# Kernel optimization log

Hardware: AMD Instinct MI355X
Metric: run time of the kernel (lower is better)

Reference implementation:

```python
import jax, jax.numpy as jnp
import numpy as np

C = 256
G = 32  # GroupNorm groups
EPS = 1e-6


def setup_inputs() -> dict:
    key = jax.random.key(0)
    ks = jax.random.split(key, 10)
    b, c, d, h, w = 2, C, 16, 16, 16
    s = 1.0 / np.sqrt(c)
    return {
        "x": jax.random.normal(ks[0], (b, c, d, h, w), jnp.float32),
        "gn_gamma": jnp.ones((c,), jnp.float32),
        "gn_beta": jnp.zeros((c,), jnp.float32),
        "wq": jax.random.normal(ks[1], (c, c), jnp.float32) * s,
        "bq": jax.random.normal(ks[2], (c,), jnp.float32) * 0.01,
        "wk": jax.random.normal(ks[3], (c, c), jnp.float32) * s,
        "bk": jax.random.normal(ks[4], (c,), jnp.float32) * 0.01,
        "wv": jax.random.normal(ks[5], (c, c), jnp.float32) * s,
        "bv": jax.random.normal(ks[6], (c,), jnp.float32) * 0.01,
        "wp": jax.random.normal(ks[7], (c, c), jnp.float32) * s,
        "bp": jax.random.normal(ks[8], (c,), jnp.float32) * 0.01,
    }


def _group_norm(x, gamma, beta):
    b, c, d, h, w = x.shape
    xg = x.reshape(b, G, c // G, d, h, w)
    mu = jnp.mean(xg, axis=(2, 3, 4, 5), keepdims=True)
    var = jnp.var(xg, axis=(2, 3, 4, 5), keepdims=True)
    xn = ((xg - mu) * jax.lax.rsqrt(var + EPS)).reshape(b, c, d, h, w)
    return xn * gamma[None, :, None, None, None] + beta[None, :, None, None, None]


def reference(x, gn_gamma, gn_beta, wq, bq, wk, bk, wv, bv, wp, bp):
    b, c, d, h, w = x.shape
    n = d * h * w
    hn = _group_norm(x, gn_gamma, gn_beta).reshape(b, c, n)  # (b, c, n)
    # 1x1 conv3d == channel-mixing matmul
    q = jnp.einsum("oc,bcn->bon", wq, hn) + bq[None, :, None]
    k = jnp.einsum("oc,bcn->bon", wk, hn) + bk[None, :, None]
    v = jnp.einsum("oc,bcn->bon", wv, hn) + bv[None, :, None]
    scale = c ** (-0.5)
    attn = jax.nn.softmax(jnp.einsum("bcn,bcm->bnm", q, k) * scale, axis=2)  # (b, n, m)
    # torch: h_ = bmm(v, attn^T) -> h_[b,c,n] = sum_m v[b,c,m] * attn[b,n,m]
    hv = jnp.einsum("bcm,bnm->bcn", v, attn)
    out = jnp.einsum("oc,bcn->bon", wp, hv) + bp[None, :, None]
    w_returned = jnp.transpose(attn, (0, 2, 1))  # matches torch's returned permuted w_
    return (x + out.reshape(b, c, d, h, w), w_returned)
```

## Files before the change

kernel.cpp:

```cpp
#include <hip/hip_runtime.h>


typedef __bf16 bf16_t;
typedef __bf16 bf16x8 __attribute__((ext_vector_type(8)));
typedef float floatx4 __attribute__((ext_vector_type(4)));

__device__ __forceinline__ unsigned short f2bf(float f) {
  union { float f; unsigned int u; } v; v.f = f;
  return (unsigned short)((v.u + 0x7FFFu + ((v.u >> 16) & 1u)) >> 16);
}
__device__ __forceinline__ float bf2f(unsigned short u) {
  union { unsigned int u; float f; } v; v.u = ((unsigned int)u) << 16;
  return v.f;
}

__global__ void conv_w_kernel(const float* __restrict__ w0, const float* __restrict__ w1,
                              const float* __restrict__ w2, const float* __restrict__ w3,
                              unsigned short* __restrict__ dst) {
  const float* src = (blockIdx.z == 0) ? w0 : (blockIdx.z == 1) ? w1 : (blockIdx.z == 2) ? w2 : w3;
  int i = blockIdx.x * 256 + threadIdx.x;
  dst[(size_t)blockIdx.z * 65536 + i] = f2bf(src[i]);
}

__global__ void pack_bias_kernel(const float* __restrict__ bq, const float* __restrict__ bk,
                                 const float* __restrict__ bv, float* __restrict__ bqkv) {
  int t = threadIdx.x;
  bqkv[t] = bq[t];
  bqkv[256 + t] = bk[t];
  bqkv[512 + t] = bv[t];
}

__global__ void gn_stats_kernel(const float* __restrict__ x, float* __restrict__ mean,
                                float* __restrict__ rstd) {
  int bg = blockIdx.x;
  const float* p = x + (size_t)bg * 32768;
  float s = 0.f, ss = 0.f;
  for (int i = threadIdx.x * 4; i < 32768; i += 1024) {
    float4 v = *(const float4*)&p[i];
    s += v.x + v.y + v.z + v.w;
    ss += v.x * v.x + v.y * v.y + v.z * v.z + v.w * v.w;
  }
  for (int off = 32; off > 0; off >>= 1) {
    s += __shfl_down(s, off);
    ss += __shfl_down(ss, off);
  }
  __shared__ float bs[4], bss[4];
  int wid = threadIdx.x >> 6;
  if ((threadIdx.x & 63) == 0) { bs[wid] = s; bss[wid] = ss; }
  __syncthreads();
  if (threadIdx.x == 0) {
    float S = bs[0] + bs[1] + bs[2] + bs[3];
    float SS = bss[0] + bss[1] + bss[2] + bss[3];
    float mu = S * (1.f / 32768.f);
    float var = SS * (1.f / 32768.f) - mu * mu;
    mean[bg] = mu;
    rstd[bg] = rsqrtf(var + 1e-6f);
  }
}

__global__ void gn_apply_t_kernel(const float* __restrict__ x, const float* __restrict__ gamma,
                                  const float* __restrict__ beta, const float* __restrict__ mean,
                                  const float* __restrict__ rstd, unsigned short* __restrict__ hnT) {
  int n0 = blockIdx.x * 64, c0 = blockIdx.y * 64, b = blockIdx.z;
  int tid = threadIdx.x;
  __shared__ __align__(16) unsigned short T[64 * 72];
#pragma unroll
  for (int r = 0; r < 4; ++r) {
    int cl = (tid >> 4) + r * 16;
    int nl = (tid & 15) * 4;
    int c = c0 + cl;
    int bg = b * 32 + (c >> 3);
    float mu = mean[bg], rs = rstd[bg], ga = gamma[c], be = beta[c];
    float4 v = *(const float4*)&x[(size_t)b * 1048576 + (size_t)c * 4096 + n0 + nl];
    ushort4 u;
    u.x = f2bf((v.x - mu) * rs * ga + be);
    u.y = f2bf((v.y - mu) * rs * ga + be);
    u.z = f2bf((v.z - mu) * rs * ga + be);
    u.w = f2bf((v.w - mu) * rs * ga + be);
    *(ushort4*)&T[cl * 72 + nl] = u;
  }
  __syncthreads();
#pragma unroll
  for (int w = 0; w < 2; ++w) {
    int nl = (tid >> 3) + w * 32;
    int cch = (tid & 7) * 8;
    unsigned short u8[8];
#pragma unroll
    for (int i = 0; i < 8; ++i) u8[i] = T[(cch + i) * 72 + nl];
    size_t o = (size_t)b * 1048576 + (size_t)(n0 + nl) * 256 + c0 + cch;
    *(ushort4*)&hnT[o] = make_ushort4(u8[0], u8[1], u8[2], u8[3]);
    *(ushort4*)&hnT[o + 4] = make_ushort4(u8[4], u8[5], u8[6], u8[7]);
  }
}

template <int BM, int BN, int MODE>
__launch_bounds__(256)
__global__ void gemm_tn(const bf16_t* __restrict__ A0, long long sA,
                        const bf16_t* __restrict__ B0, long long sB, int ldb,
                        void* __restrict__ C0, long long sC,
                        const float* __restrict__ bias, int M, int N, int K) {
  constexpr int BK = 32, LD = BK + 8;
  constexpr int WM = BM / 2, WN = BN / 2, MI = WM / 16, NI = WN / 16;
  __shared__ __align__(16) bf16_t As[BM * LD];
  __shared__ __align__(16) bf16_t Bs[BN * LD];
  const int tid = threadIdx.x;
  const int lane = tid & 63, wid = tid >> 6;
  const int quad = lane >> 4, l16 = lane & 15;
  const int bz = blockIdx.z;
  const bf16_t* A = A0 + (size_t)bz * sA;
  const bf16_t* B = B0 + (size_t)bz * sB;
  const int m0 = blockIdx.y * BM, n0 = blockIdx.x * BN;
  const int wm0 = (wid >> 1) * WM, wn0 = (wid & 1) * WN;

  floatx4 acc[MI][NI];
#pragma unroll
  for (int i = 0; i < MI; ++i)
#pragma unroll
    for (int j = 0; j < NI; ++j) acc[i][j] = (floatx4){0.f, 0.f, 0.f, 0.f};

  const int arow = tid >> 2, akj = (tid & 3) << 3;
  for (int kt = 0; kt < K; kt += BK) {
#pragma unroll
    for (int p = 0; p < BM / 64; ++p) {
      int r = p * 64 + arow;
      *(uint4*)&As[r * LD + akj] = *(const uint4*)&A[(size_t)(m0 + r) * K + kt + akj];
    }
#pragma unroll
    for (int p = 0; p < BN / 64; ++p) {
      int r = p * 64 + arow;
      *(uint4*)&Bs[r * LD + akj] = *(const uint4*)&B[(size_t)(n0 + r) * ldb + kt + akj];
    }
    __syncthreads();
    bf16x8 af[MI], bfr[NI];
#pragma unroll
    for (int i = 0; i < MI; ++i) af[i] = *(const bf16x8*)&As[(wm0 + i * 16 + l16) * LD + quad * 8];
#pragma unroll
    for (int j = 0; j < NI; ++j) bfr[j] = *(const bf16x8*)&Bs[(wn0 + j * 16 + l16) * LD + quad * 8];
#pragma unroll
    for (int i = 0; i < MI; ++i)
#pragma unroll
      for (int j = 0; j < NI; ++j)
        acc[i][j] = __builtin_amdgcn_mfma_f32_16x16x32_bf16(af[i], bfr[j], acc[i][j], 0, 0, 0);
    __syncthreads();
  }

#pragma unroll
  for (int i = 0; i < MI; ++i) {
    int gmb = m0 + wm0 + i * 16 + quad * 4;
#pragma unroll
    for (int j = 0; j < NI; ++j) {
      int gn = n0 + wn0 + j * 16 + l16;
      float v[4];
#pragma unroll
      for (int r = 0; r < 4; ++r) v[r] = acc[i][j][r];
      if (bias != nullptr) {
#pragma unroll
        for (int r = 0; r < 4; ++r) v[r] += bias[gmb + r];
      }
      if (MODE == 2) {
        unsigned short* Cb = (unsigned short*)C0 + (size_t)bz * sC;
#pragma unroll
        for (int r = 0; r < 4; ++r) Cb[(size_t)(gmb + r) * N + gn] = f2bf(v[r]);
      } else {
        unsigned short* Cb = (unsigned short*)C0 + (size_t)bz * sC;
        ushort4 u = make_ushort4(f2bf(v[0]), f2bf(v[1]), f2bf(v[2]), f2bf(v[3]));
        *(ushort4*)&Cb[(size_t)gn * M + gmb] = u;
      }
    }
  }
}

__launch_bounds__(256)
__global__ void gemm_qk_exp(const bf16_t* __restrict__ qkvT, unsigned short* __restrict__ EbfT,
                            float* __restrict__ psum) {
  constexpr int BM = 128, BN = 128, BK = 32, LD = BK + 8, MI = 4, NI = 4;
  constexpr int LDC = BM + 8;
  __shared__ __align__(16) char SMEM[BM * LDC * 2];
  bf16_t* As = (bf16_t*)SMEM;
  bf16_t* Bs = (bf16_t*)SMEM + BM * LD;
  unsigned short* Ct = (unsigned short*)SMEM;
  const int tid = threadIdx.x;
  const int lane = tid & 63, wid = tid >> 6;
  const int quad = lane >> 4, l16 = lane & 15;
  const int b = blockIdx.z;
  const bf16_t* A = qkvT + (size_t)b * 3145728 + 256;
  const bf16_t* B = qkvT + (size_t)b * 3145728;
  const int m0 = blockIdx.y * BM, n0 = blockIdx.x * BN;
  const int wm0 = (wid >> 1) * 64, wn0 = (wid & 1) * 64;

  floatx4 acc[MI][NI];
#pragma unroll
  for (int i = 0; i < MI; ++i)
#pragma unroll
    for (int j = 0; j < NI; ++j) acc[i][j] = (floatx4){0.f, 0.f, 0.f, 0.f};

  const int arow = tid >> 2, akj = (tid & 3) << 3;
  for (int kt = 0; kt < 256; kt += BK) {
#pragma unroll
    for (int p = 0; p < 2; ++p) {
      int r = p * 64 + arow;
      *(uint4*)&As[r * LD + akj] = *(const uint4*)&A[(size_t)(m0 + r) * 768 + kt + akj];
      *(uint4*)&Bs[r * LD + akj] = *(const uint4*)&B[(size_t)(n0 + r) * 768 + kt + akj];
    }
    __syncthreads();
    bf16x8 af[MI], bfr[NI];
#pragma unroll
    for (int i = 0; i < MI; ++i) af[i] = *(const bf16x8*)&As[(wm0 + i * 16 + l16) * LD + quad * 8];
#pragma unroll
    for (int j = 0; j < NI; ++j) bfr[j] = *(const bf16x8*)&Bs[(wn0 + j * 16 + l16) * LD + quad * 8];
#pragma unroll
    for (int i = 0; i < MI; ++i)
#pragma unroll
      for (int j = 0; j < NI; ++j)
        acc[i][j] = __builtin_amdgcn_mfma_f32_16x16x32_bf16(af[i], bfr[j], acc[i][j], 0, 0, 0);
    __syncthreads();
  }

  float csum[NI] = {0.f, 0.f, 0.f, 0.f};
#pragma unroll
  for (int i = 0; i < MI; ++i) {
    int ml = wm0 + i * 16 + quad * 4;
#pragma unroll
    for (int j = 0; j < NI; ++j) {
      int nl = wn0 + j * 16 + l16;
      float e[4];
#pragma unroll
      for (int r = 0; r < 4; ++r) e[r] = __expf(acc[i][j][r] * 0.0625f);
      csum[j] += (e[0] + e[1]) + (e[2] + e[3]);
      *(ushort4*)&Ct[nl * LDC + ml] = make_ushort4(f2bf(e[0]), f2bf(e[1]), f2bf(e[2]), f2bf(e[3]));
    }
  }
#pragma unroll
  for (int j = 0; j < NI; ++j) {
    csum[j] += __shfl_xor(csum[j], 16);
    csum[j] += __shfl_xor(csum[j], 32);
  }
  if (quad == 0) {
    int my = blockIdx.y * 2 + (wid >> 1);
#pragma unroll
    for (int j = 0; j < NI; ++j)
      psum[((size_t)b * 64 + my) * 4096 + n0 + wn0 + j * 16 + l16] = csum[j];
  }
  __syncthreads();
#pragma unroll
  for (int pass = 0; pass < 8; ++pass) {
    int row = pass * 16 + (tid >> 4);
    int mc = (tid & 15) * 8;
    uint4 v = *(uint4*)&Ct[row * LDC + mc];
    *(uint4*)&EbfT[(size_t)b * 16777216 + (size_t)(n0 + row) * 4096 + m0 + mc] = v;
  }
}

__global__ void combine_kernel(const float* __restrict__ psum, float* __restrict__ rsum) {
  int b = blockIdx.y;
  int n = blockIdx.x * 256 + threadIdx.x;
  float s = 0.f;
#pragma unroll
  for (int r = 0; r < 64; ++r) s += psum[((size_t)b * 64 + r) * 4096 + n];
  rsum[b * 4096 + n] = 1.f / s;
}

__launch_bounds__(512)
__global__ void gemm_pv_fused(const bf16_t* __restrict__ W2, const bf16_t* __restrict__ EbfT,
                              const float* __restrict__ rsum, float* __restrict__ attn,
                              float* __restrict__ part0, float* __restrict__ part1) {
  constexpr int BK = 32, LD = BK + 8;
  __shared__ __align__(16) bf16_t As[256 * LD];
  __shared__ __align__(16) bf16_t Bs[64 * LD];
  __shared__ float rs[64];
  const int tid = threadIdx.x;
  const int lane = tid & 63, wid = tid >> 6;
  const int quad = lane >> 4, l16 = lane & 15;
  const int kb = blockIdx.y, b = blockIdx.z;
  const int n0 = blockIdx.x * 64;
  const size_t eb = (size_t)b * 16777216;
  if (tid < 64) rs[tid] = rsum[b * 4096 + n0 + tid];
  __syncthreads();
  const int wm0 = (wid >> 1) * 64, wn0 = (wid & 1) * 32;

  floatx4 acc[4][2];
#pragma unroll
  for (int i = 0; i < 4; ++i)
#pragma unroll
    for (int j = 0; j < 2; ++j) acc[i][j] = (floatx4){0.f, 0.f, 0.f, 0.f};

  const int ar = tid >> 2, ak = (tid & 3) << 3;
  for (int kt = 0; kt < 2048; kt += BK) {
    const int gm = kb * 2048 + kt;
#pragma unroll
    for (int p = 0; p < 2; ++p) {
      int r = p * 128 + ar;
      *(uint4*)&As[r * LD + ak] =
          *(const uint4*)&W2[(size_t)b * 1048576 + (size_t)r * 4096 + gm + ak];
    }
    if (tid < 256) {
      int r = tid >> 2;
      int kk = (tid & 3) << 3;
      *(uint4*)&Bs[r * LD + kk] = *(const uint4*)&EbfT[eb + (size_t)(n0 + r) * 4096 + gm + kk];
    }
    __syncthreads();
    {
      int ml = tid >> 4;
      int n4 = (tid & 15) * 4;
      const unsigned short* Bu = (const unsigned short*)Bs;
      float4 o;
      o.x = bf2f(Bu[(n4 + 0) * LD + ml]) * rs[n4 + 0];
      o.y = bf2f(Bu[(n4 + 1) * LD + ml]) * rs[n4 + 1];
      o.z = bf2f(Bu[(n4 + 2) * LD + ml]) * rs[n4 + 2];
      o.w = bf2f(Bu[(n4 + 3) * LD + ml]) * rs[n4 + 3];
      *(float4*)&attn[eb + (size_t)(gm + ml) * 4096 + n0 + n4] = o;
    }
    bf16x8 af[4], bfr[2];
#pragma unroll
    for (int i = 0; i < 4; ++i) af[i] = *(const bf16x8*)&As[(wm0 + i * 16 + l16) * LD + quad * 8];
#pragma unroll
    for (int j = 0; j < 2; ++j) bfr[j] = *(const bf16x8*)&Bs[(wn0 + j * 16 + l16) * LD + quad * 8];
#pragma unroll
    for (int i = 0; i < 4; ++i)
#pragma unroll
      for (int j = 0; j < 2; ++j)
        acc[i][j] = __builtin_amdgcn_mfma_f32_16x16x32_bf16(af[i], bfr[j], acc[i][j], 0, 0, 0);
    __syncthreads();
  }

  float* part = kb ? part1 : part0;
#pragma unroll
  for (int i = 0; i < 4; ++i) {
    int row = wm0 + i * 16 + quad * 4;
#pragma unroll
    for (int j = 0; j < 2; ++j) {
      int cl = wn0 + j * 16 + l16;
      float cs = rs[cl];
#pragma unroll
      for (int r = 0; r < 4; ++r)
        part[(size_t)b * 1048576 + (size_t)(row + r) * 4096 + n0 + cl] = acc[i][j][r] * cs;
    }
  }
}

__global__ void reduce_kernel(float* __restrict__ out0, const float* __restrict__ part1,
                              const float* __restrict__ bp, const float* __restrict__ x) {
  size_t idx = ((size_t)blockIdx.x * 256 + threadIdx.x) * 4;
  int o = (int)((idx >> 12) & 255);
  float4 a = *(float4*)&out0[idx];
  float4 p = *(const float4*)&part1[idx];
  float4 xr = *(const float4*)&x[idx];
  float bb = bp[o];
  a.x += p.x + xr.x + bb;
  a.y += p.y + xr.y + bb;
  a.z += p.z + xr.z + bb;
  a.w += p.w + xr.w + bb;
  *(float4*)&out0[idx] = a;
}

extern "C" void kernel_launch(void* const* d_in, const int* in_sizes, int n_in,
                              void* d_out, int out_size, void* d_ws, size_t ws_size,
                              hipStream_t stream) {
  const float* x = (const float*)d_in[0];
  const float* gamma = (const float*)d_in[1];
  const float* beta = (const float*)d_in[2];
  const float* wq = (const float*)d_in[3];
  const float* bq = (const float*)d_in[4];
  const float* wk = (const float*)d_in[5];
  const float* bk = (const float*)d_in[6];
  const float* wv = (const float*)d_in[7];
  const float* bv = (const float*)d_in[8];
  const float* wp = (const float*)d_in[9];
  const float* bp = (const float*)d_in[10];

  float* out0 = (float*)d_out;
  float* attn = (float*)d_out + 2097152;

  char* ws = (char*)d_ws;
  unsigned short* wbf = (unsigned short*)(ws + 0);
  float* bqkv = (float*)(ws + 524288);
  float* gmean = (float*)(ws + 528384);
  float* grstd = (float*)(ws + 528640);
  float* psum = (float*)(ws + 1048576);
  float* rsum = (float*)(ws + 3145728);
  unsigned short* hnT = (unsigned short*)(ws + 4194304);
  unsigned short* W2 = (unsigned short*)(ws + 4194304);
  unsigned short* qkvT = (unsigned short*)(ws + 8388608);
  float* part1 = (float*)(ws + 8388608);
  unsigned short* EbfT = (unsigned short*)(ws + 20971520);

  conv_w_kernel<<<dim3(256, 1, 4), 256, 0, stream>>>(wq, wk, wv, wp, wbf);
  pack_bias_kernel<<<1, 256, 0, stream>>>(bq, bk, bv, bqkv);
  gn_stats_kernel<<<64, 256, 0, stream>>>(x, gmean, grstd);
  gn_apply_t_kernel<<<dim3(64, 4, 2), 256, 0, stream>>>(x, gamma, beta, gmean, grstd, hnT);

  gemm_tn<64, 128, 3><<<dim3(32, 12, 2), 256, 0, stream>>>(
      (const bf16_t*)wbf, 0, (const bf16_t*)hnT, 1048576, 256, qkvT, 3145728, bqkv, 768, 4096, 256);

  gemm_tn<64, 128, 2><<<dim3(32, 4, 2), 256, 0, stream>>>(
      (const bf16_t*)(wbf + 196608), 0, (const bf16_t*)qkvT + 512, 3145728, 768, W2, 1048576,
      nullptr, 256, 4096, 256);

  gemm_qk_exp<<<dim3(32, 32, 2), 256, 0, stream>>>((const bf16_t*)qkvT, EbfT, psum);
  combine_kernel<<<dim3(16, 2), 256, 0, stream>>>(psum, rsum);

  gemm_pv_fused<<<dim3(64, 2, 2), 512, 0, stream>>>((const bf16_t*)W2, (const bf16_t*)EbfT, rsum,
                                                    attn, out0, part1);
  reduce_kernel<<<2048, 256, 0, stream>>>(out0, part1, bp, x);
}
```

Measured before the change: 314.6 us.

## Fold projection weight into V, merge prep kernels, fuse softmax-normalize and residual into PV

Precomputes Wp·Wv as a combined weight, so the V projection GEMM produces W2 = (Wp·Wv)·hn directly and the separate projection GEMM disappears. Bias folding moves Wp·bv + bp into a single bias2 vector. The setup kernels (weight conversion, bias packing, GN stats) merge into one prep kernel. The row-sum combine and the final reduce kernel are absorbed into the PV kernel, which now sums psum itself and writes out = acc*rs + bias2 + x directly without a split-K partial buffer. This trades fewer launches and less intermediate traffic for extra bf16 rounding from the folded weight and a different PV tiling.

Result: faster. 277.8 us (-11.7%).

```diff
diff --git a/kernel.cpp b/kernel.cpp
--- a/kernel.cpp
+++ b/kernel.cpp
@@ -14,47 +14,78 @@
   return v.f;
 }
 
-__global__ void conv_w_kernel(const float* __restrict__ w0, const float* __restrict__ w1,
-                              const float* __restrict__ w2, const float* __restrict__ w3,
-                              unsigned short* __restrict__ dst) {
-  const float* src = (blockIdx.z == 0) ? w0 : (blockIdx.z == 1) ? w1 : (blockIdx.z == 2) ? w2 : w3;
-  int i = blockIdx.x * 256 + threadIdx.x;
-  dst[(size_t)blockIdx.z * 65536 + i] = f2bf(src[i]);
-}
-
-__global__ void pack_bias_kernel(const float* __restrict__ bq, const float* __restrict__ bk,
-                                 const float* __restrict__ bv, float* __restrict__ bqkv) {
-  int t = threadIdx.x;
-  bqkv[t] = bq[t];
-  bqkv[256 + t] = bk[t];
-  bqkv[512 + t] = bv[t];
-}
-
-__global__ void gn_stats_kernel(const float* __restrict__ x, float* __restrict__ mean,
-                                float* __restrict__ rstd) {
-  int bg = blockIdx.x;
-  const float* p = x + (size_t)bg * 32768;
-  float s = 0.f, ss = 0.f;
-  for (int i = threadIdx.x * 4; i < 32768; i += 1024) {
-    float4 v = *(const float4*)&p[i];
-    s += v.x + v.y + v.z + v.w;
-    ss += v.x * v.x + v.y * v.y + v.z * v.z + v.w * v.w;
-  }
-  for (int off = 32; off > 0; off >>= 1) {
-    s += __shfl_down(s, off);
-    ss += __shfl_down(ss, off);
-  }
-  __shared__ float bs[4], bss[4];
-  int wid = threadIdx.x >> 6;
-  if ((threadIdx.x & 63) == 0) { bs[wid] = s; bss[wid] = ss; }
-  __syncthreads();
-  if (threadIdx.x == 0) {
-    float S = bs[0] + bs[1] + bs[2] + bs[3];
-    float SS = bss[0] + bss[1] + bss[2] + bss[3];
-    float mu = S * (1.f / 32768.f);
-    float var = SS * (1.f / 32768.f) - mu * mu;
-    mean[bg] = mu;
-    rstd[bg] = rsqrtf(var + 1e-6f);
+__global__ void prep_kernel(const float* __restrict__ wq, const float* __restrict__ wk,
+                            const float* __restrict__ wv, const float* __restrict__ wp,
+                            const float* __restrict__ bq, const float* __restrict__ bk,
+                            const float* __restrict__ bv, const float* __restrict__ bp,
+                            const float* __restrict__ x, unsigned short* __restrict__ Astack,
+                            unsigned short* __restrict__ wpbf, unsigned short* __restrict__ wvT,
+                            float* __restrict__ bqkv2, float* __restrict__ bias2,
+                            float* __restrict__ mean, float* __restrict__ rstd) {
+  __shared__ float T[64 * 67];
+  __shared__ float red[256];
+  const int blk = blockIdx.x;
+  const int tid = threadIdx.x;
+  if (blk < 768) {
+    int w = blk >> 8;
+    const float* src = (w == 0) ? wq : (w == 1) ? wk : wp;
+    unsigned short* dst = (w == 0) ? Astack : (w == 1) ? (Astack + 65536) : wpbf;
+    int i = (blk & 255) * 256 + tid;
+    dst[i] = f2bf(src[i]);
+  } else if (blk < 784) {
+    int t = blk - 768, tr = t >> 2, tc = t & 3;
+#pragma unroll
+    for (int rr = 0; rr < 16; ++rr) {
+      int r = rr * 4 + (tid >> 6), c = tid & 63;
+      T[r * 67 + c] = wv[(size_t)(tr * 64 + r) * 256 + tc * 64 + c];
+    }
+    __syncthreads();
+#pragma unroll
+    for (int rr = 0; rr < 16; ++rr) {
+      int cc = rr * 4 + (tid >> 6), r = tid & 63;
+      wvT[(size_t)(tc * 64 + cc) * 256 + tr * 64 + r] = f2bf(T[r * 67 + cc]);
+    }
+  } else if (blk < 848) {
+    int bg = blk - 784;
+    const float* p = x + (size_t)bg * 32768;
+    float s = 0.f, ss = 0.f;
+    for (int i = tid * 4; i < 32768; i += 1024) {
+      float4 v = *(const float4*)&p[i];
+      s += v.x + v.y + v.z + v.w;
+      ss += v.x * v.x + v.y * v.y + v.z * v.z + v.w * v.w;
+    }
+    for (int off = 32; off > 0; off >>= 1) {
+      s += __shfl_down(s, off);
+      ss += __shfl_down(ss, off);
+    }
+    int wid = tid >> 6;
+    if ((tid & 63) == 0) { red[wid] = s; red[64 + wid] = ss; }
+    __syncthreads();
+    if (tid == 0) {
+      float S = red[0] + red[1] + red[2] + red[3];
+      float SS = red[64] + red[65] + red[66] + red[67];
+      float mu = S * (1.f / 32768.f);
+      float var = SS * (1.f / 32768.f) - mu * mu;
+      mean[bg] = mu;
+      rstd[bg] = rsqrtf(var + 1e-6f);
+    }
+  } else if (blk == 848) {
+    bqkv2[tid] = bq[tid];
+    bqkv2[256 + tid] = bk[tid];
+    bqkv2[512 + tid] = 0.f;
+  } else {
+    int bb = blk - 849;
+    int o = bb * 64 + (tid >> 2), part = tid & 3;
+    float s = 0.f;
+#pragma unroll
+    for (int j = 0; j < 16; ++j) {
+      float4 w4 = *(const float4*)&wp[(size_t)o * 256 + part * 64 + j * 4];
+      float4 b4 = *(const float4*)&bv[part * 64 + j * 4];
+      s += w4.x * b4.x + w4.y * b4.y + w4.z * b4.z + w4.w * b4.w;
+    }
+    red[tid] = s;
+    __syncthreads();
+    if (part == 0) bias2[o] = bp[o] + red[tid] + red[tid + 1] + red[tid + 2] + red[tid + 3];
   }
 }
 
@@ -93,12 +124,10 @@
   }
 }
 
-template <int BM, int BN, int MODE>
+template <int BM, int BN>
 __launch_bounds__(256)
-__global__ void gemm_tn(const bf16_t* __restrict__ A0, long long sA,
-                        const bf16_t* __restrict__ B0, long long sB, int ldb,
-                        void* __restrict__ C0, long long sC,
-                        const float* __restrict__ bias, int M, int N, int K) {
+__global__ void gemm_tn(const bf16_t* __restrict__ A, const bf16_t* __restrict__ B, int ldb,
+                        unsigned short* __restrict__ C, int N, int K) {
   constexpr int BK = 32, LD = BK + 8;
   constexpr int WM = BM / 2, WN = BN / 2, MI = WM / 16, NI = WN / 16;
   __shared__ __align__(16) bf16_t As[BM * LD];
@@ -106,9 +135,6 @@
   const int tid = threadIdx.x;
   const int lane = tid & 63, wid = tid >> 6;
   const int quad = lane >> 4, l16 = lane & 15;
-  const int bz = blockIdx.z;
-  const bf16_t* A = A0 + (size_t)bz * sA;
-  const bf16_t* B = B0 + (size_t)bz * sB;
   const int m0 = blockIdx.y * BM, n0 = blockIdx.x * BN;
   const int wm0 = (wid >> 1) * WM, wn0 = (wid & 1) * WN;
 
@@ -150,28 +176,81 @@
 #pragma unroll
     for (int j = 0; j < NI; ++j) {
       int gn = n0 + wn0 + j * 16 + l16;
+#pragma unroll
+      for (int r = 0; r < 4; ++r) C[(size_t)(gmb + r) * N + gn] = f2bf(acc[i][j][r]);
+    }
+  }
+}
+
+__launch_bounds__(256)
+__global__ void gemm_qkvw(const bf16_t* __restrict__ Astack, const bf16_t* __restrict__ hnT,
+                          const float* __restrict__ bqkv2, unsigned short* __restrict__ qkT,
+                          unsigned short* __restrict__ W2) {
+  constexpr int BM = 64, BN = 128, BK = 32, LD = BK + 8, MI = 2, NI = 4;
+  __shared__ __align__(16) bf16_t As[BM * LD];
+  __shared__ __align__(16) bf16_t Bs[BN * LD];
+  const int tid = threadIdx.x;
+  const int lane = tid & 63, wid = tid >> 6;
+  const int quad = lane >> 4, l16 = lane & 15;
+  const int b = blockIdx.z;
+  const bf16_t* B = hnT + (size_t)b * 1048576;
+  const int m0 = blockIdx.y * BM, n0 = blockIdx.x * BN;
+  const int wm0 = (wid >> 1) * 32, wn0 = (wid & 1) * 64;
+
+  floatx4 acc[MI][NI];
+#pragma unroll
+  for (int i = 0; i < MI; ++i)
+#pragma unroll
+    for (int j = 0; j < NI; ++j) acc[i][j] = (floatx4){0.f, 0.f, 0.f, 0.f};
+
+  const int arow = tid >> 2, akj = (tid & 3) << 3;
+  for (int kt = 0; kt < 256; kt += BK) {
+    {
+      int r = arow;
+      *(uint4*)&As[r * LD + akj] = *(const uint4*)&Astack[(size_t)(m0 + r) * 256 + kt + akj];
+    }
+#pragma unroll
+    for (int p = 0; p < 2; ++p) {
+      int r = p * 64 + arow;
+      *(uint4*)&Bs[r * LD + akj] = *(const uint4*)&B[(size_t)(n0 + r) * 256 + kt + akj];
+    }
+    __syncthreads();
+    bf16x8 af[MI], bfr[NI];
+#pragma unroll
+    for (int i = 0; i < MI; ++i) af[i] = *(const bf16x8*)&As[(wm0 + i * 16 + l16) * LD + quad * 8];
+#pragma unroll
+    for (int j = 0; j < NI; ++j) bfr[j] = *(const bf16x8*)&Bs[(wn0 + j * 16 + l16) * LD + quad * 8];
+#pragma unroll
+    for (int i = 0; i < MI; ++i)
+#pragma unroll
+      for (int j = 0; j < NI; ++j)
+        acc[i][j] = __builtin_amdgcn_mfma_f32_16x16x32_bf16(af[i], bfr[j], acc[i][j], 0, 0, 0);
+    __syncthreads();
+  }
+
+#pragma unroll
+  for (int i = 0; i < MI; ++i) {
+    int gmb = m0 + wm0 + i * 16 + quad * 4;
+#pragma unroll
+    for (int j = 0; j < NI; ++j) {
+      int gn = n0 + wn0 + j * 16 + l16;
       float v[4];
 #pragma unroll
-      for (int r = 0; r < 4; ++r) v[r] = acc[i][j][r];
-      if (bias != nullptr) {
-#pragma unroll
-        for (int r = 0; r < 4; ++r) v[r] += bias[gmb + r];
+      for (int r = 0; r < 4; ++r) v[r] = acc[i][j][r] + bqkv2[gmb + r];
+      if (m0 < 512) {
+        ushort4 u = make_ushort4(f2bf(v[0]), f2bf(v[1]), f2bf(v[2]), f2bf(v[3]));
+        *(ushort4*)&qkT[(size_t)b * 2097152 + (size_t)gn * 512 + gmb] = u;
+      } else {
+#pragma unroll
+        for (int r = 0; r < 4; ++r)
+          W2[(size_t)b * 1048576 + (size_t)(gmb - 512 + r) * 4096 + gn] = f2bf(v[r]);
       }
-      if (MODE == 2) {
-        unsigned short* Cb = (unsigned short*)C0 + (size_t)bz * sC;
-#pragma unroll
-        for (int r = 0; r < 4; ++r) Cb[(size_t)(gmb + r) * N + gn] = f2bf(v[r]);
-      } else {
-        unsigned short* Cb = (unsigned short*)C0 + (size_t)bz * sC;
-        ushort4 u = make_ushort4(f2bf(v[0]), f2bf(v[1]), f2bf(v[2]), f2bf(v[3]));
-        *(ushort4*)&Cb[(size_t)gn * M + gmb] = u;
-      }
     }
   }
 }
 
 __launch_bounds__(256)
-__global__ void gemm_qk_exp(const bf16_t* __restrict__ qkvT, unsigned short* __restrict__ EbfT,
+__global__ void gemm_qk_exp(const bf16_t* __restrict__ qkT, unsigned short* __restrict__ EbfT,
                             float* __restrict__ psum) {
   constexpr int BM = 128, BN = 128, BK = 32, LD = BK + 8, MI = 4, NI = 4;
   constexpr int LDC = BM + 8;
@@ -183,8 +262,8 @@
   const int lane = tid & 63, wid = tid >> 6;
   const int quad = lane >> 4, l16 = lane & 15;
   const int b = blockIdx.z;
-  const bf16_t* A = qkvT + (size_t)b * 3145728 + 256;
-  const bf16_t* B = qkvT + (size_t)b * 3145728;
+  const bf16_t* A = qkT + (size_t)b * 2097152 + 256;
+  const bf16_t* B = qkT + (size_t)b * 2097152;
   const int m0 = blockIdx.y * BM, n0 = blockIdx.x * BN;
   const int wm0 = (wid >> 1) * 64, wn0 = (wid & 1) * 64;
 
@@ -199,8 +278,8 @@
 #pragma unroll
     for (int p = 0; p < 2; ++p) {
       int r = p * 64 + arow;
-      *(uint4*)&As[r * LD + akj] = *(const uint4*)&A[(size_t)(m0 + r) * 768 + kt + akj];
-      *(uint4*)&Bs[r * LD + akj] = *(const uint4*)&B[(size_t)(n0 + r) * 768 + kt + akj];
+      *(uint4*)&As[r * LD + akj] = *(const uint4*)&A[(size_t)(m0 + r) * 512 + kt + akj];
+      *(uint4*)&Bs[r * LD + akj] = *(const uint4*)&B[(size_t)(n0 + r) * 512 + kt + akj];
     }
     __syncthreads();
     bf16x8 af[MI], bfr[NI];
@@ -251,106 +330,97 @@
   }
 }
 
-__global__ void combine_kernel(const float* __restrict__ psum, float* __restrict__ rsum) {
-  int b = blockIdx.y;
-  int n = blockIdx.x * 256 + threadIdx.x;
-  float s = 0.f;
-#pragma unroll
-  for (int r = 0; r < 64; ++r) s += psum[((size_t)b * 64 + r) * 4096 + n];
-  rsum[b * 4096 + n] = 1.f / s;
-}
-
-__launch_bounds__(512)
+__launch_bounds__(256)
 __global__ void gemm_pv_fused(const bf16_t* __restrict__ W2, const bf16_t* __restrict__ EbfT,
-                              const float* __restrict__ rsum, float* __restrict__ attn,
-                              float* __restrict__ part0, float* __restrict__ part1) {
-  constexpr int BK = 32, LD = BK + 8;
-  __shared__ __align__(16) bf16_t As[256 * LD];
-  __shared__ __align__(16) bf16_t Bs[64 * LD];
-  __shared__ float rs[64];
+                              const float* __restrict__ psum, const float* __restrict__ bias2,
+                              const float* __restrict__ x, float* __restrict__ out0,
+                              float* __restrict__ attn) {
+  constexpr int BK = 64, LDA = 72, LDB = 72;
+  __shared__ __align__(16) bf16_t As[128 * LDA];
+  __shared__ __align__(16) bf16_t Bs[32 * LDB];
+  __shared__ float rs[32];
+  __shared__ float sred[256];
   const int tid = threadIdx.x;
   const int lane = tid & 63, wid = tid >> 6;
   const int quad = lane >> 4, l16 = lane & 15;
-  const int kb = blockIdx.y, b = blockIdx.z;
-  const int n0 = blockIdx.x * 64;
+  const int b = blockIdx.z, mb = blockIdx.y;
+  const int n0 = blockIdx.x * 32;
   const size_t eb = (size_t)b * 16777216;
-  if (tid < 64) rs[tid] = rsum[b * 4096 + n0 + tid];
+
+  {
+    int nl = tid & 31, rp = tid >> 5;
+    float s = 0.f;
+#pragma unroll
+    for (int i = 0; i < 8; ++i) s += psum[((size_t)b * 64 + rp * 8 + i) * 4096 + n0 + nl];
+    sred[tid] = s;
+  }
   __syncthreads();
-  const int wm0 = (wid >> 1) * 64, wn0 = (wid & 1) * 32;
-
-  floatx4 acc[4][2];
-#pragma unroll
-  for (int i = 0; i < 4; ++i)
-#pragma unroll
-    for (int j = 0; j < 2; ++j) acc[i][j] = (floatx4){0.f, 0.f, 0.f, 0.f};
-
-  const int ar = tid >> 2, ak = (tid & 3) << 3;
-  for (int kt = 0; kt < 2048; kt += BK) {
-    const int gm = kb * 2048 + kt;
-#pragma unroll
-    for (int p = 0; p < 2; ++p) {
-      int r = p * 128 + ar;
-      *(uint4*)&As[r * LD + ak] =
-          *(const uint4*)&W2[(size_t)b * 1048576 + (size_t)r * 4096 + gm + ak];
-    }
-    if (tid < 256) {
-      int r = tid >> 2;
-      int kk = (tid & 3) << 3;
-      *(uint4*)&Bs[r * LD + kk] = *(const uint4*)&EbfT[eb + (size_t)(n0 + r) * 4096 + gm + kk];
-    }
-    __syncthreads();
+  if (tid < 32) {
+    float s = 0.f;
+#pragma unroll
+    for (int i = 0; i < 8; ++i) s += sred[i * 32 + tid];
+    rs[tid] = 1.f / s;
+  }
+  __syncthreads();
+
+  const int wm0 = (wid >> 1) * 64, wn0 = (wid & 1) * 16;
+  floatx4 acc[4];
+#pragma unroll
+  for (int i = 0; i < 4; ++i) acc[i] = (floatx4){0.f, 0.f, 0.f, 0.f};
+
+  for (int kt = 0; kt < 4096; kt += BK) {
+#pragma unroll
+    for (int p = 0; p < 4; ++p) {
+      int r = p * 32 + (tid >> 3);
+      int kk = (tid & 7) * 8;
+      *(uint4*)&As[r * LDA + kk] =
+          *(const uint4*)&W2[(size_t)b * 1048576 + (size_t)(mb * 128 + r) * 4096 + kt + kk];
+    }
     {
-      int ml = tid >> 4;
-      int n4 = (tid & 15) * 4;
+      int r = tid >> 3;
+      int kk = (tid & 7) * 8;
+      *(uint4*)&Bs[r * LDB + kk] = *(const uint4*)&EbfT[eb + (size_t)(n0 + r) * 4096 + kt + kk];
+    }
+    __syncthreads();
+    {
+      int ml = mb * 32 + (tid >> 3);
+      int n4 = (tid & 7) * 4;
       const unsigned short* Bu = (const unsigned short*)Bs;
       float4 o;
-      o.x = bf2f(Bu[(n4 + 0) * LD + ml]) * rs[n4 + 0];
-      o.y = bf2f(Bu[(n4 + 1) * LD + ml]) * rs[n4 + 1];
-      o.z = bf2f(Bu[(n4 + 2) * LD + ml]) * rs[n4 + 2];
-      o.w = bf2f(Bu[(n4 + 3) * LD + ml]) * rs[n4 + 3];
-      *(float4*)&attn[eb + (size_t)(gm + ml) * 4096 + n0 + n4] = o;
-    }
-    bf16x8 af[4], bfr[2];
-#pragma unroll
-    for (int i = 0; i < 4; ++i) af[i] = *(const bf16x8*)&As[(wm0 + i * 16 + l16) * LD + quad * 8];
-#pragma unroll
-    for (int j = 0; j < 2; ++j) bfr[j] = *(const bf16x8*)&Bs[(wn0 + j * 16 + l16) * LD + quad * 8];
-#pragma unroll
-    for (int i = 0; i < 4; ++i)
-#pragma unroll
-      for (int j = 0; j < 2; ++j)
-        acc[i][j] = __builtin_amdgcn_mfma_f32_16x16x32_bf16(af[i], bfr[j], acc[i][j], 0, 0, 0);
-    __syncthreads();
-  }
-
-  float* part = kb ? part1 : part0;
+      o.x = bf2f(Bu[(n4 + 0) * LDB + ml]) * rs[n4 + 0];
+      o.y = bf2f(Bu[(n4 + 1) * LDB + ml]) * rs[n4 + 1];
+      o.z = bf2f(Bu[(n4 + 2) * LDB + ml]) * rs[n4 + 2];
+      o.w = bf2f(Bu[(n4 + 3) * LDB + ml]) * rs[n4 + 3];
+      *(float4*)&attn[eb + (size_t)(kt + ml) * 4096 + n0 + n4] = o;
+    }
+    bf16x8 af[2][4], bfr[2];
+#pragma unroll
+    for (int ks = 0; ks < 2; ++ks) {
+      bfr[ks] = *(const bf16x8*)&Bs[(wn0 + l16) * LDB + ks * 32 + quad * 8];
+#pragma unroll
+      for (int i = 0; i < 4; ++i)
+        af[ks][i] = *(const bf16x8*)&As[(wm0 + i * 16 + l16) * LDA + ks * 32 + quad * 8];
+    }
+#pragma unroll
+    for (int ks = 0; ks < 2; ++ks)
+#pragma unroll
+      for (int i = 0; i < 4; ++i)
+        acc[i] = __builtin_amdgcn_mfma_f32_16x16x32_bf16(af[ks][i], bfr[ks], acc[i], 0, 0, 0);
+    __syncthreads();
+  }
+
+  const float* xb = x + (size_t)b * 1048576;
+  float* ob = out0 + (size_t)b * 1048576;
+  int gn = n0 + wn0 + l16;
+  float cs = rs[wn0 + l16];
 #pragma unroll
   for (int i = 0; i < 4; ++i) {
-    int row = wm0 + i * 16 + quad * 4;
-#pragma unroll
-    for (int j = 0; j < 2; ++j) {
-      int cl = wn0 + j * 16 + l16;
-      float cs = rs[cl];
-#pragma unroll
-      for (int r = 0; r < 4; ++r)
-        part[(size_t)b * 1048576 + (size_t)(row + r) * 4096 + n0 + cl] = acc[i][j][r] * cs;
-    }
-  }
-}
-
-__global__ void reduce_kernel(float* __restrict__ out0, const float* __restrict__ part1,
-                              const float* __restrict__ bp, const float* __restrict__ x) {
-  size_t idx = ((size_t)blockIdx.x * 256 + threadIdx.x) * 4;
-  int o = (int)((idx >> 12) & 255);
-  float4 a = *(float4*)&out0[idx];
-  float4 p = *(const float4*)&part1[idx];
-  float4 xr = *(const float4*)&x[idx];
-  float bb = bp[o];
-  a.x += p.x + xr.x + bb;
-  a.y += p.y + xr.y + bb;
-  a.z += p.z + xr.z + bb;
-  a.w += p.w + xr.w + bb;
-  *(float4*)&out0[idx] = a;
+    int o = mb * 128 + wm0 + i * 16 + quad * 4;
+#pragma unroll
+    for (int r = 0; r < 4; ++r)
+      ob[(size_t)(o + r) * 4096 + gn] =
+          acc[i][r] * cs + bias2[o + r] + xb[(size_t)(o + r) * 4096 + gn];
+  }
 }
 
 extern "C" void kernel_launch(void* const* d_in, const int* in_sizes, int n_in,
@@ -372,34 +442,32 @@
   float* attn = (float*)d_out + 2097152;
 
   char* ws = (char*)d_ws;
-  unsigned short* wbf = (unsigned short*)(ws + 0);
-  float* bqkv = (float*)(ws + 524288);
-  float* gmean = (float*)(ws + 528384);
-  float* grstd = (float*)(ws + 528640);
+  unsigned short* Astack = (unsigned short*)(ws + 0);
+  unsigned short* wpbf = (unsigned short*)(ws + 393216);
+  unsigned short* wvT = (unsigned short*)(ws + 524288);
+  float* bqkv2 = (float*)(ws + 655360);
+  float* bias2 = (float*)(ws + 658432);
+  float* gmean = (float*)(ws + 659456);
+  float* grstd = (float*)(ws + 659712);
   float* psum = (float*)(ws + 1048576);
-  float* rsum = (float*)(ws + 3145728);
   unsigned short* hnT = (unsigned short*)(ws + 4194304);
-  unsigned short* W2 = (unsigned short*)(ws + 4194304);
-  unsigned short* qkvT = (unsigned short*)(ws + 8388608);
-  float* part1 = (float*)(ws + 8388608);
+  unsigned short* qkT = (unsigned short*)(ws + 8388608);
+  unsigned short* W2 = (unsigned short*)(ws + 16777216);
   unsigned short* EbfT = (unsigned short*)(ws + 20971520);
 
-  conv_w_kernel<<<dim3(256, 1, 4), 256, 0, stream>>>(wq, wk, wv, wp, wbf);
-  pack_bias_kernel<<<1, 256, 0, stream>>>(bq, bk, bv, bqkv);
-  gn_stats_kernel<<<64, 256, 0, stream>>>(x, gmean, grstd);
+  prep_kernel<<<853, 256, 0, stream>>>(wq, wk, wv, wp, bq, bk, bv, bp, x, Astack, wpbf, wvT,
+                                       bqkv2, bias2, gmean, grstd);
+
+  gemm_tn<64, 128><<<dim3(2, 4, 1), 256, 0, stream>>>((const bf16_t*)wpbf, (const bf16_t*)wvT, 256,
+                                                      Astack + 131072, 256, 256);
+
   gn_apply_t_kernel<<<dim3(64, 4, 2), 256, 0, stream>>>(x, gamma, beta, gmean, grstd, hnT);
 
-  gemm_tn<64, 128, 3><<<dim3(32, 12, 2), 256, 0, stream>>>(
-      (const bf16_t*)wbf, 0, (const bf16_t*)hnT, 1048576, 256, qkvT, 3145728, bqkv, 768, 4096, 256);
-
-  gemm_tn<64, 128, 2><<<dim3(32, 4, 2), 256, 0, stream>>>(
-      (const bf16_t*)(wbf + 196608), 0, (const bf16_t*)qkvT + 512, 3145728, 768, W2, 1048576,
-      nullptr, 256, 4096, 256);
-
-  gemm_qk_exp<<<dim3(32, 32, 2), 256, 0, stream>>>((const bf16_t*)qkvT, EbfT, psum);
-  combine_kernel<<<dim3(16, 2), 256, 0, stream>>>(psum, rsum);
-
-  gemm_pv_fused<<<dim3(64, 2, 2), 512, 0, stream>>>((const bf16_t*)W2, (const bf16_t*)EbfT, rsum,
-                                                    attn, out0, part1);
-  reduce_kernel<<<2048, 256, 0, stream>>>(out0, part1, bp, x);
-}
+  gemm_qkvw<<<dim3(32, 12, 2), 256, 0, stream>>>((const bf16_t*)Astack, (const bf16_t*)hnT, bqkv2,
+                                                 qkT, W2);
+
+  gemm_qk_exp<<<dim3(32, 32, 2), 256, 0, stream>>>((const bf16_t*)qkT, EbfT, psum);
+
+  gemm_pv_fused<<<dim3(128, 2, 2), 256, 0, stream>>>((const bf16_t*)W2, (const bf16_t*)EbfT, psum,
+                                                     bias2, x, out0, attn);
+}
```
